# Kernel tuning notes

Measured on AMD Instinct MI355X. Metric: run time of the kernel, lower is better.

Reference implementation:

```python
import jax, jax.numpy as jnp
import numpy as np

NSAMPLE = 3  # three_nn default
EPS = 1e-10
CLAMP = 10.0


def setup_inputs() -> dict:
    key = jax.random.key(0)
    k1, k2, k3 = jax.random.split(key, 3)
    B, C, N = 4, 3, 8192
    pos1 = jax.random.normal(k1, (B, C, N), dtype=jnp.float32)
    pos2 = jax.random.normal(k2, (B, C, N), dtype=jnp.float32)
    flow1 = jax.random.normal(k3, (B, C, N), dtype=jnp.float32) * 0.1
    return {"pos1": pos1, "pos2": pos2, "flow1": flow1}


def reference(pos1, pos2, flow1):
    # pos1, flow1: [B,3,N1]; pos2: [B,3,N2]
    pos1_to_2 = pos1 + flow1                       # warped source points [B,3,N1]
    q = jnp.transpose(pos2, (0, 2, 1))             # queries  [B,N2,3]
    k = jnp.transpose(pos1_to_2, (0, 2, 1))        # database [B,N1,3]

    # brute-force 3-NN: squared distances [B,N2,N1]
    d2 = (jnp.sum(q * q, axis=-1, keepdims=True)
          - 2.0 * jnp.einsum('bqc,bnc->bqn', q, k)
          + jnp.sum(k * k, axis=-1)[:, None, :])
    _, knn_idx = jax.lax.top_k(-d2, NSAMPLE)       # [B,N2,NSAMPLE] into N1

    # gather neighbor coords: [B,N2,NSAMPLE,3]
    grouped_pts = jax.vmap(lambda pts, ii: pts[ii])(k, knn_idx)
    diff = grouped_pts - q[:, :, None, :]
    dist = jnp.maximum(jnp.linalg.norm(diff, axis=-1), EPS)  # [B,N2,NSAMPLE]
    inv = 1.0 / dist
    weight = inv / jnp.sum(inv, axis=-1, keepdims=True)      # [B,N2,NSAMPLE]

    # gather neighbor flows and do inverse-distance-weighted average
    flow_t = jnp.transpose(flow1, (0, 2, 1))                 # [B,N1,3]
    grouped_flow = jax.vmap(lambda f, ii: f[ii])(flow_t, knn_idx)  # [B,N2,NSAMPLE,3]
    flow2 = jnp.sum(weight[..., None] * grouped_flow, axis=2)      # [B,N2,3]

    warped = pos2 - jnp.transpose(flow2, (0, 2, 1))          # [B,3,N2]
    return jnp.clip(warped, -CLAMP, CLAMP)
```

## Files before the change

### kernel.cpp

```cpp
#include <hip/hip_runtime.h>
#include <math.h>


#define BB 4
#define NN 8192
#define NC 30
#define NCELLS (NC * NC * NC)
#define NCT (BB * NCELLS)
#define GRID_R 3.3f
#define GRID_INVH (1.0f / 0.22f)
#define D3_THR (0.44f * 0.44f * 0.999f)
#define EPB 1024
#define SB 106
#define NZ4 ((NCT + 4) / 4)

typedef unsigned long long u64;

__device__ __forceinline__ int cell_of(float x) {
  int c = (int)floorf((x + GRID_R) * GRID_INVH);
  return min(max(c, 0), NC - 1);
}

__device__ __forceinline__ void merge3(u64& a0, u64& a1, u64& a2,
                                       u64 b0, u64 b1, u64 b2) {
  const u64 lo0 = a0 < b0 ? a0 : b0;
  const u64 hi0 = a0 < b0 ? b0 : a0;
  const u64 lo1 = a1 < b1 ? a1 : b1;
  const u64 lo2 = a2 < b2 ? a2 : b2;
  const u64 o1 = hi0 < lo1 ? hi0 : lo1;
  const u64 t = hi0 < lo1 ? lo1 : hi0;
  a0 = lo0;
  a1 = o1;
  a2 = t < lo2 ? t : lo2;
}

__device__ __forceinline__ void insert3(u64& s0, u64& s1, u64& s2, u64 key) {
  const bool c0 = key < s0;
  const bool c1 = key < s1;
  const bool c2 = key < s2;
  s2 = c1 ? s1 : (c2 ? key : s2);
  s1 = c0 ? s0 : (c1 ? key : s1);
  s0 = c0 ? key : s0;
}

__device__ __forceinline__ void wave_merge3(u64& s0, u64& s1, u64& s2) {
#pragma unroll
  for (int mask = 32; mask >= 1; mask >>= 1) {
    const u64 b0 = __shfl_xor(s0, mask, 64);
    const u64 b1 = __shfl_xor(s1, mask, 64);
    const u64 b2 = __shfl_xor(s2, mask, 64);
    merge3(s0, s1, s2, b0, b1, b2);
  }
}

__device__ __forceinline__ void idw_out(int b, int qn, float qx, float qy,
                                        float qz, u64 s0, u64 s1, u64 s2,
                                        const float* __restrict__ P1,
                                        const float* __restrict__ F1,
                                        float* __restrict__ out) {
  const int idxs[3] = {(int)(unsigned)s0 & (NN - 1),
                       (int)(unsigned)s1 & (NN - 1),
                       (int)(unsigned)s2 & (NN - 1)};
  float w[3], gfx[3], gfy[3], gfz[3];
  float wsumv = 0.0f;
#pragma unroll
  for (int r = 0; r < 3; ++r) {
    const int idx = idxs[r];
    const float fx = F1[idx], fy = F1[NN + idx], fz = F1[2 * NN + idx];
    const float kx = P1[idx] + fx;
    const float ky = P1[NN + idx] + fy;
    const float kz = P1[2 * NN + idx] + fz;
    const float dx = kx - qx, dy = ky - qy, dz = kz - qz;
    float d = sqrtf(dx * dx + dy * dy + dz * dz);
    d = fmaxf(d, 1e-10f);
    const float inv = 1.0f / d;
    w[r] = inv; wsumv += inv;
    gfx[r] = fx; gfy[r] = fy; gfz[r] = fz;
  }
  const float invw = 1.0f / wsumv;
  float ox = 0.0f, oy = 0.0f, oz = 0.0f;
#pragma unroll
  for (int r = 0; r < 3; ++r) {
    const float ww = w[r] * invw;
    ox = fmaf(ww, gfx[r], ox);
    oy = fmaf(ww, gfy[r], oy);
    oz = fmaf(ww, gfz[r], oz);
  }
  ox = qx - ox; oy = qy - oy; oz = qz - oz;
  ox = fminf(fmaxf(ox, -10.0f), 10.0f);
  oy = fminf(fmaxf(oy, -10.0f), 10.0f);
  oz = fminf(fmaxf(oz, -10.0f), 10.0f);
  float* o = out + (size_t)b * 3 * NN;
  o[qn] = ox;
  o[NN + qn] = oy;
  o[2 * NN + qn] = oz;
}

__global__ __launch_bounds__(256) void k_zero(int4* __restrict__ p) {
  const int i = blockIdx.x * 256 + threadIdx.x;
  if (i < NZ4) p[i] = make_int4(0, 0, 0, 0);
}

__global__ __launch_bounds__(256) void k_count(const float* __restrict__ p1,
                                               const float* __restrict__ f1,
                                               int* __restrict__ counts) {
  const int gid = blockIdx.x * 256 + threadIdx.x;
  const int b = gid >> 13, n = gid & (NN - 1);
  const float* P = p1 + (size_t)b * 3 * NN;
  const float* F = f1 + (size_t)b * 3 * NN;
  const float x = P[n] + F[n];
  const float y = P[NN + n] + F[NN + n];
  const float z = P[2 * NN + n] + F[2 * NN + n];
  const int cid = (cell_of(z) * NC + cell_of(y)) * NC + cell_of(x);
  atomicAdd(&counts[b * NCELLS + cid], 1);
}

__global__ __launch_bounds__(256) void k_scan1(int* __restrict__ counts,
                                               int* __restrict__ offs,
                                               int* __restrict__ partials) {
  __shared__ int wsums[4];
  const int tid = threadIdx.x, lane = tid & 63, wav = tid >> 6;
  const int c = blockIdx.x * EPB + tid * 4;
  int4 v = make_int4(0, 0, 0, 0);
  if (c < NCT) {
    v = *reinterpret_cast<const int4*>(counts + c);
    *reinterpret_cast<int4*>(counts + c) = make_int4(0, 0, 0, 0);
  }
  const int sum4 = v.x + v.y + v.z + v.w;
  int incl = sum4;
  for (int off = 1; off < 64; off <<= 1) {
    const int t = __shfl_up(incl, off, 64);
    incl += (lane >= off) ? t : 0;
  }
  if (lane == 63) wsums[wav] = incl;
  __syncthreads();
  int wbase = 0;
#pragma unroll
  for (int w = 0; w < 4; ++w) wbase += (w < wav) ? wsums[w] : 0;
  const int excl = wbase + incl - sum4;
  if (c < NCT) {
    int4 e;
    e.x = excl;
    e.y = excl + v.x;
    e.z = e.y + v.y;
    e.w = e.z + v.z;
    *reinterpret_cast<int4*>(offs + c) = e;
  }
  if (tid == 255) partials[blockIdx.x] = wbase + incl;
}

__global__ __launch_bounds__(256) void k_finalize(int* __restrict__ offs,
                                                  const int* __restrict__ partials) {
  __shared__ int sbase;
  const int tid = threadIdx.x, lane = tid & 63;
  const int bid = blockIdx.x;
  if (tid < 64) {
    int v = 0;
    if (lane < bid) v = partials[lane];
    if (lane + 64 < bid) v += partials[lane + 64];
    for (int off = 32; off >= 1; off >>= 1) v += __shfl_down(v, off, 64);
    if (lane == 0) sbase = v;
  }
  __syncthreads();
  const int base = sbase;
  const int c = bid * EPB + tid * 4;
  if (c < NCT) {
    int4 v = *reinterpret_cast<const int4*>(offs + c);
    v.x += base; v.y += base; v.z += base; v.w += base;
    *reinterpret_cast<int4*>(offs + c) = v;
  }
  if (bid == 0 && tid == 0) offs[NCT] = BB * NN;
}

__global__ __launch_bounds__(256) void k_scatter(const float* __restrict__ p1,
                                                 const float* __restrict__ f1,
                                                 int* __restrict__ counts,
                                                 const int* __restrict__ offs,
                                                 float4* __restrict__ csr) {
  const int gid = blockIdx.x * 256 + threadIdx.x;
  const int b = gid >> 13, n = gid & (NN - 1);
  const float* P = p1 + (size_t)b * 3 * NN;
  const float* F = f1 + (size_t)b * 3 * NN;
  const float x = P[n] + F[n];
  const float y = P[NN + n] + F[NN + n];
  const float z = P[2 * NN + n] + F[2 * NN + n];
  const int cid = (cell_of(z) * NC + cell_of(y)) * NC + cell_of(x);
  const int g = b * NCELLS + cid;
  const int rank = atomicAdd(&counts[g], 1);
  csr[offs[g] + rank] = make_float4(x, y, z, __int_as_float(n));
}

__device__ __forceinline__ void col_range(int c, int qcy, int qcz, int cb,
                                          int gxl, int span,
                                          const int* __restrict__ offs,
                                          int& st, int& en) {
  const int dzi = (c * 205) >> 10;
  const int gz = qcz + dzi - 2;
  const int gy = qcy + (c - dzi * 5) - 2;
  st = 0; en = 0;
  if (((unsigned)gz < NC) & ((unsigned)gy < NC)) {
    const int ia = cb + (gz * NC + gy) * NC + gxl;
    st = offs[ia];
    en = offs[ia + span];
  }
}

__device__ __forceinline__ void cand1(const float4& a, float qx, float qy,
                                      float qz, u64& s0, u64& s1, u64& s2) {
  const float dx = a.x - qx, dy = a.y - qy, dz = a.z - qz;
  const float d2 = fmaf(dx, dx, fmaf(dy, dy, dz * dz));
  insert3(s0, s1, s2,
          ((u64)__float_as_uint(d2) << 32) | (unsigned)__float_as_uint(a.w));
}

__device__ __forceinline__ void scan_col(int st, int en,
                                         const float4* __restrict__ csr,
                                         float qx, float qy, float qz,
                                         u64& s0, u64& s1, u64& s2) {
  int j = st;
  for (; j + 4 <= en; j += 4) {
    const float4 a = csr[j];
    const float4 b = csr[j + 1];
    const float4 c = csr[j + 2];
    const float4 d = csr[j + 3];
    cand1(a, qx, qy, qz, s0, s1, s2);
    cand1(b, qx, qy, qz, s0, s1, s2);
    cand1(c, qx, qy, qz, s0, s1, s2);
    cand1(d, qx, qy, qz, s0, s1, s2);
  }
  for (; j < en; ++j) {
    const float4 a = csr[j];
    cand1(a, qx, qy, qz, s0, s1, s2);
  }
}

__global__ __launch_bounds__(256) void k_query(const float* __restrict__ p1,
                                               const float* __restrict__ p2,
                                               const float* __restrict__ f1,
                                               const int* __restrict__ offs,
                                               const float4* __restrict__ csr,
                                               float* __restrict__ out,
                                               int* __restrict__ fbcnt,
                                               int* __restrict__ fbq) {
  const int gtid = blockIdx.x * 256 + threadIdx.x;
  const int qid = gtid >> 4;
  const int r = gtid & 15;
  const int b = qid >> 13;
  const int qn = qid & (NN - 1);
  const float* P1 = p1 + (size_t)b * 3 * NN;
  const float* P2 = p2 + (size_t)b * 3 * NN;
  const float* F1 = f1 + (size_t)b * 3 * NN;

  const float qx = P2[qn], qy = P2[NN + qn], qz = P2[2 * NN + qn];
  const bool oor = !(fabsf(qx) < GRID_R && fabsf(qy) < GRID_R && fabsf(qz) < GRID_R);

  u64 s0 = ~0ULL, s1 = ~0ULL, s2 = ~0ULL;

  if (!oor) {
    const int qcx = cell_of(qx), qcy = cell_of(qy), qcz = cell_of(qz);
    const int gxl = max(qcx - 2, 0);
    const int span = min(qcx + 2, NC - 1) - gxl + 1;
    const int cb = b * NCELLS;

    int st0, en0, st1 = 0, en1 = 0;
    col_range(r, qcy, qcz, cb, gxl, span, offs, st0, en0);
    if (r < 9) col_range(r + 16, qcy, qcz, cb, gxl, span, offs, st1, en1);

    scan_col(st0, en0, csr, qx, qy, qz, s0, s1, s2);
    scan_col(st1, en1, csr, qx, qy, qz, s0, s1, s2);
  }

#pragma unroll
  for (int mask = 1; mask <= 8; mask <<= 1) {
    const u64 b0 = __shfl_xor(s0, mask, 64);
    const u64 b1 = __shfl_xor(s1, mask, 64);
    const u64 b2 = __shfl_xor(s2, mask, 64);
    merge3(s0, s1, s2, b0, b1, b2);
  }

  if (r == 0) {
    const float d3 = __uint_as_float((unsigned)(s2 >> 32));
    const bool ok = !oor && (d3 <= D3_THR);
    if (!ok) {
      const int slot = atomicAdd(&fbcnt[b], 1);
      fbq[b * NN + slot] = qn;
    } else {
      idw_out(b, qn, qx, qy, qz, s0, s1, s2, P1, F1, out);
    }
  }
}

__global__ __launch_bounds__(256) void k_fallback(const float* __restrict__ p1,
                                                  const float* __restrict__ p2,
                                                  const float* __restrict__ f1,
                                                  const int* __restrict__ fbcnt,
                                                  const int* __restrict__ fbq,
                                                  float* __restrict__ out) {
  __shared__ u64 redA[4][3];
  __shared__ u64 redC[4][3];
  const int b = blockIdx.y;
  const int nfb = fbcnt[b];
  const int tid = threadIdx.x, lane = tid & 63, wav = tid >> 6;
  const float* P1 = p1 + (size_t)b * 3 * NN;
  const float* P2 = p2 + (size_t)b * 3 * NN;
  const float* F1 = f1 + (size_t)b * 3 * NN;
  const int* q = fbq + b * NN;

  for (int base = blockIdx.x * 2; base < nfb; base += gridDim.x * 2) {
    const bool v1 = base + 1 < nfb;
    const int qn0 = q[base] & (NN - 1);
    const int qn1 = (v1 ? q[base + 1] : q[base]) & (NN - 1);
    const float q0x = P2[qn0], q0y = P2[NN + qn0], q0z = P2[2 * NN + qn0];
    const float q1x = P2[qn1], q1y = P2[NN + qn1], q1z = P2[2 * NN + qn1];

    u64 a0 = ~0ULL, a1 = ~0ULL, a2 = ~0ULL;
    u64 c0 = ~0ULL, c1 = ~0ULL, c2 = ~0ULL;

    for (int g0 = 0; g0 < NN; g0 += 1024) {
      const int g = g0 + tid;
      float xs[4], ys[4], zs[4];
#pragma unroll
      for (int k = 0; k < 4; ++k) {
        const int gg = g + k * 256;
        xs[k] = P1[gg] + F1[gg];
        ys[k] = P1[NN + gg] + F1[NN + gg];
        zs[k] = P1[2 * NN + gg] + F1[2 * NN + gg];
      }
#pragma unroll
      for (int k = 0; k < 4; ++k) {
        const unsigned gg = (unsigned)(g + k * 256);
        {
          const float dx = xs[k] - q0x, dy = ys[k] - q0y, dz = zs[k] - q0z;
          const float d2 = fmaf(dx, dx, fmaf(dy, dy, dz * dz));
          insert3(a0, a1, a2, ((u64)__float_as_uint(d2) << 32) | gg);
        }
        {
          const float dx = xs[k] - q1x, dy = ys[k] - q1y, dz = zs[k] - q1z;
          const float d2 = fmaf(dx, dx, fmaf(dy, dy, dz * dz));
          insert3(c0, c1, c2, ((u64)__float_as_uint(d2) << 32) | gg);
        }
      }
    }

    wave_merge3(a0, a1, a2);
    wave_merge3(c0, c1, c2);
    if (lane == 0) {
      redA[wav][0] = a0; redA[wav][1] = a1; redA[wav][2] = a2;
      redC[wav][0] = c0; redC[wav][1] = c1; redC[wav][2] = c2;
    }
    __syncthreads();
    if (tid == 0) {
      u64 m0 = redA[0][0], m1 = redA[0][1], m2 = redA[0][2];
#pragma unroll
      for (int w = 1; w < 4; ++w) merge3(m0, m1, m2, redA[w][0], redA[w][1], redA[w][2]);
      idw_out(b, qn0, q0x, q0y, q0z, m0, m1, m2, P1, F1, out);
    }
    if (tid == 1 && v1) {
      u64 m0 = redC[0][0], m1 = redC[0][1], m2 = redC[0][2];
#pragma unroll
      for (int w = 1; w < 4; ++w) merge3(m0, m1, m2, redC[w][0], redC[w][1], redC[w][2]);
      idw_out(b, qn1, q1x, q1y, q1z, m0, m1, m2, P1, F1, out);
    }
    __syncthreads();
  }
}

extern "C" void kernel_launch(void* const* d_in, const int* in_sizes, int n_in,
                              void* d_out, int out_size, void* d_ws, size_t ws_size,
                              hipStream_t stream) {
  const float* pos1 = (const float*)d_in[0];
  const float* pos2 = (const float*)d_in[1];
  const float* flow1 = (const float*)d_in[2];
  float* out = (float*)d_out;

  char* ws = (char*)d_ws;
  int* counts = (int*)ws;
  int* fbcnt = counts + NCT;
  size_t offs_off = (((size_t)NCT + 4) * 4 + 15) & ~(size_t)15;
  int* offs = (int*)(ws + offs_off);
  size_t part_off = (offs_off + ((size_t)NCT + 1) * 4 + 15) & ~(size_t)15;
  int* partials = (int*)(ws + part_off);
  size_t fbq_off = (part_off + (size_t)SB * 4 + 15) & ~(size_t)15;
  int* fbq = (int*)(ws + fbq_off);
  size_t csr_off = (fbq_off + (size_t)BB * NN * 4 + 15) & ~(size_t)15;
  float4* csr = (float4*)(ws + csr_off);

  k_zero<<<dim3((NZ4 + 255) / 256), dim3(256), 0, stream>>>((int4*)counts);
  k_count<<<dim3(BB * NN / 256), dim3(256), 0, stream>>>(pos1, flow1, counts);
  k_scan1<<<dim3(SB), dim3(256), 0, stream>>>(counts, offs, partials);
  k_finalize<<<dim3(SB), dim3(256), 0, stream>>>(offs, partials);
  k_scatter<<<dim3(BB * NN / 256), dim3(256), 0, stream>>>(pos1, flow1, counts, offs, csr);
  k_query<<<dim3(BB * NN * 16 / 256), dim3(256), 0, stream>>>(pos1, pos2, flow1, offs, csr, out, fbcnt, fbq);
  k_fallback<<<dim3(128, BB), dim3(256), 0, stream>>>(pos1, pos2, flow1, fbcnt, fbq, out);
}
```

Baseline: 70.97 us.

## Sort queries by grid cell so neighboring threads share CSR cells

Query points are binned into the same spatial grid as the database points through a shared count/scan/scatter pipeline, which produces a cell-sorted query list. k_query now reads its query id from this list, so adjacent waves process spatially nearby queries. The aim is better cache locality and less divergence in loop trip counts during the cell scans. The cost is a doubled scan array, more work in the count and scatter kernels, and an extra indirection per query.

Result: slower. 72.50 us (+2.1%).

```diff
diff --git a/kernel.cpp b/kernel.cpp
--- a/kernel.cpp
+++ b/kernel.cpp
@@ -4,15 +4,17 @@
 
 #define BB 4
 #define NN 8192
+#define BBNN (BB * NN)
 #define NC 30
 #define NCELLS (NC * NC * NC)
 #define NCT (BB * NCELLS)
+#define NCT2 (2 * NCT)
 #define GRID_R 3.3f
 #define GRID_INVH (1.0f / 0.22f)
 #define D3_THR (0.44f * 0.44f * 0.999f)
 #define EPB 1024
-#define SB 106
-#define NZ4 ((NCT + 4) / 4)
+#define SB 211
+#define NZ4 (NCT2 / 4 + 1)
 
 typedef unsigned long long u64;
 
@@ -51,6 +53,14 @@
     const u64 b2 = __shfl_xor(s2, mask, 64);
     merge3(s0, s1, s2, b0, b1, b2);
   }
+}
+
+__device__ __forceinline__ void cand1(const float4& a, float qx, float qy,
+                                      float qz, u64& s0, u64& s1, u64& s2) {
+  const float dx = a.x - qx, dy = a.y - qy, dz = a.z - qz;
+  const float d2 = fmaf(dx, dx, fmaf(dy, dy, dz * dz));
+  insert3(s0, s1, s2,
+          ((u64)__float_as_uint(d2) << 32) | (unsigned)__float_as_uint(a.w));
 }
 
 __device__ __forceinline__ void idw_out(int b, int qn, float qx, float qy,
@@ -102,17 +112,25 @@
 }
 
 __global__ __launch_bounds__(256) void k_count(const float* __restrict__ p1,
+                                               const float* __restrict__ p2,
                                                const float* __restrict__ f1,
                                                int* __restrict__ counts) {
   const int gid = blockIdx.x * 256 + threadIdx.x;
-  const int b = gid >> 13, n = gid & (NN - 1);
-  const float* P = p1 + (size_t)b * 3 * NN;
-  const float* F = f1 + (size_t)b * 3 * NN;
-  const float x = P[n] + F[n];
-  const float y = P[NN + n] + F[NN + n];
-  const float z = P[2 * NN + n] + F[2 * NN + n];
+  const bool isq = gid >= BBNN;
+  const int id = isq ? gid - BBNN : gid;
+  const int b = id >> 13, n = id & (NN - 1);
+  float x, y, z;
+  if (isq) {
+    const float* P = p2 + (size_t)b * 3 * NN;
+    x = P[n]; y = P[NN + n]; z = P[2 * NN + n];
+  } else {
+    const float* P = p1 + (size_t)b * 3 * NN;
+    const float* F = f1 + (size_t)b * 3 * NN;
+    x = P[n] + F[n]; y = P[NN + n] + F[NN + n]; z = P[2 * NN + n] + F[2 * NN + n];
+  }
   const int cid = (cell_of(z) * NC + cell_of(y)) * NC + cell_of(x);
-  atomicAdd(&counts[b * NCELLS + cid], 1);
+  const int g = (isq ? NCT : 0) + b * NCELLS + cid;
+  atomicAdd(&counts[g], 1);
 }
 
 __global__ __launch_bounds__(256) void k_scan1(int* __restrict__ counts,
@@ -122,7 +140,7 @@
   const int tid = threadIdx.x, lane = tid & 63, wav = tid >> 6;
   const int c = blockIdx.x * EPB + tid * 4;
   int4 v = make_int4(0, 0, 0, 0);
-  if (c < NCT) {
+  if (c < NCT2) {
     v = *reinterpret_cast<const int4*>(counts + c);
     *reinterpret_cast<int4*>(counts + c) = make_int4(0, 0, 0, 0);
   }
@@ -138,7 +156,7 @@
 #pragma unroll
   for (int w = 0; w < 4; ++w) wbase += (w < wav) ? wsums[w] : 0;
   const int excl = wbase + incl - sum4;
-  if (c < NCT) {
+  if (c < NCT2) {
     int4 e;
     e.x = excl;
     e.y = excl + v.x;
@@ -149,45 +167,58 @@
   if (tid == 255) partials[blockIdx.x] = wbase + incl;
 }
 
-__global__ __launch_bounds__(256) void k_finalize(int* __restrict__ offs,
-                                                  const int* __restrict__ partials) {
+__global__ __launch_bounds__(256) void k_final(int* __restrict__ offs,
+                                               const int* __restrict__ partials) {
   __shared__ int sbase;
   const int tid = threadIdx.x, lane = tid & 63;
   const int bid = blockIdx.x;
   if (tid < 64) {
     int v = 0;
-    if (lane < bid) v = partials[lane];
-    if (lane + 64 < bid) v += partials[lane + 64];
+#pragma unroll
+    for (int k = 0; k < 4; ++k) {
+      const int j = lane + 64 * k;
+      if (j < bid) v += partials[j];
+    }
     for (int off = 32; off >= 1; off >>= 1) v += __shfl_down(v, off, 64);
     if (lane == 0) sbase = v;
   }
   __syncthreads();
   const int base = sbase;
   const int c = bid * EPB + tid * 4;
-  if (c < NCT) {
+  if (c < NCT2) {
     int4 v = *reinterpret_cast<const int4*>(offs + c);
     v.x += base; v.y += base; v.z += base; v.w += base;
     *reinterpret_cast<int4*>(offs + c) = v;
   }
-  if (bid == 0 && tid == 0) offs[NCT] = BB * NN;
-}
-
-__global__ __launch_bounds__(256) void k_scatter(const float* __restrict__ p1,
-                                                 const float* __restrict__ f1,
-                                                 int* __restrict__ counts,
-                                                 const int* __restrict__ offs,
-                                                 float4* __restrict__ csr) {
+  if (bid == 0 && tid == 0) offs[NCT2] = 2 * BBNN;
+}
+
+__global__ __launch_bounds__(256) void k_scat(const float* __restrict__ p1,
+                                              const float* __restrict__ p2,
+                                              const float* __restrict__ f1,
+                                              int* __restrict__ counts,
+                                              const int* __restrict__ offs,
+                                              float4* __restrict__ csr,
+                                              int* __restrict__ qlist) {
   const int gid = blockIdx.x * 256 + threadIdx.x;
-  const int b = gid >> 13, n = gid & (NN - 1);
-  const float* P = p1 + (size_t)b * 3 * NN;
-  const float* F = f1 + (size_t)b * 3 * NN;
-  const float x = P[n] + F[n];
-  const float y = P[NN + n] + F[NN + n];
-  const float z = P[2 * NN + n] + F[2 * NN + n];
+  const bool isq = gid >= BBNN;
+  const int id = isq ? gid - BBNN : gid;
+  const int b = id >> 13, n = id & (NN - 1);
+  float x, y, z;
+  if (isq) {
+    const float* P = p2 + (size_t)b * 3 * NN;
+    x = P[n]; y = P[NN + n]; z = P[2 * NN + n];
+  } else {
+    const float* P = p1 + (size_t)b * 3 * NN;
+    const float* F = f1 + (size_t)b * 3 * NN;
+    x = P[n] + F[n]; y = P[NN + n] + F[NN + n]; z = P[2 * NN + n] + F[2 * NN + n];
+  }
   const int cid = (cell_of(z) * NC + cell_of(y)) * NC + cell_of(x);
-  const int g = b * NCELLS + cid;
+  const int g = (isq ? NCT : 0) + b * NCELLS + cid;
   const int rank = atomicAdd(&counts[g], 1);
-  csr[offs[g] + rank] = make_float4(x, y, z, __int_as_float(n));
+  const int pos = offs[g] + rank;
+  if (isq) qlist[pos - BBNN] = id;
+  else csr[pos] = make_float4(x, y, z, __int_as_float(n));
 }
 
 __device__ __forceinline__ void col_range(int c, int qcy, int qcz, int cb,
@@ -203,14 +234,6 @@
     st = offs[ia];
     en = offs[ia + span];
   }
-}
-
-__device__ __forceinline__ void cand1(const float4& a, float qx, float qy,
-                                      float qz, u64& s0, u64& s1, u64& s2) {
-  const float dx = a.x - qx, dy = a.y - qy, dz = a.z - qz;
-  const float d2 = fmaf(dx, dx, fmaf(dy, dy, dz * dz));
-  insert3(s0, s1, s2,
-          ((u64)__float_as_uint(d2) << 32) | (unsigned)__float_as_uint(a.w));
 }
 
 __device__ __forceinline__ void scan_col(int st, int en,
@@ -239,12 +262,14 @@
                                                const float* __restrict__ f1,
                                                const int* __restrict__ offs,
                                                const float4* __restrict__ csr,
+                                               const int* __restrict__ qlist,
                                                float* __restrict__ out,
                                                int* __restrict__ fbcnt,
                                                int* __restrict__ fbq) {
   const int gtid = blockIdx.x * 256 + threadIdx.x;
-  const int qid = gtid >> 4;
+  const int e = gtid >> 4;
   const int r = gtid & 15;
+  const int qid = qlist[e];
   const int b = qid >> 13;
   const int qn = qid & (NN - 1);
   const float* P1 = p1 + (size_t)b * 3 * NN;
@@ -375,21 +400,25 @@
 
   char* ws = (char*)d_ws;
   int* counts = (int*)ws;
-  int* fbcnt = counts + NCT;
-  size_t offs_off = (((size_t)NCT + 4) * 4 + 15) & ~(size_t)15;
+  int* fbcnt = counts + NCT2;
+  size_t offs_off = (((size_t)NCT2 + 4) * 4 + 15) & ~(size_t)15;
   int* offs = (int*)(ws + offs_off);
-  size_t part_off = (offs_off + ((size_t)NCT + 1) * 4 + 15) & ~(size_t)15;
+  size_t part_off = (offs_off + ((size_t)NCT2 + 1) * 4 + 15) & ~(size_t)15;
   int* partials = (int*)(ws + part_off);
-  size_t fbq_off = (part_off + (size_t)SB * 4 + 15) & ~(size_t)15;
+  size_t ql_off = (part_off + (size_t)SB * 4 + 15) & ~(size_t)15;
+  int* qlist = (int*)(ws + ql_off);
+  size_t fbq_off = (ql_off + (size_t)BBNN * 4 + 15) & ~(size_t)15;
   int* fbq = (int*)(ws + fbq_off);
-  size_t csr_off = (fbq_off + (size_t)BB * NN * 4 + 15) & ~(size_t)15;
+  size_t csr_off = (fbq_off + (size_t)BBNN * 4 + 15) & ~(size_t)15;
   float4* csr = (float4*)(ws + csr_off);
 
   k_zero<<<dim3((NZ4 + 255) / 256), dim3(256), 0, stream>>>((int4*)counts);
-  k_count<<<dim3(BB * NN / 256), dim3(256), 0, stream>>>(pos1, flow1, counts);
+  k_count<<<dim3(2 * BBNN / 256), dim3(256), 0, stream>>>(pos1, pos2, flow1, counts);
   k_scan1<<<dim3(SB), dim3(256), 0, stream>>>(counts, offs, partials);
-  k_finalize<<<dim3(SB), dim3(256), 0, stream>>>(offs, partials);
-  k_scatter<<<dim3(BB * NN / 256), dim3(256), 0, stream>>>(pos1, flow1, counts, offs, csr);
-  k_query<<<dim3(BB * NN * 16 / 256), dim3(256), 0, stream>>>(pos1, pos2, flow1, offs, csr, out, fbcnt, fbq);
+  k_final<<<dim3(SB), dim3(256), 0, stream>>>(offs, partials);
+  k_scat<<<dim3(2 * BBNN / 256), dim3(256), 0, stream>>>(pos1, pos2, flow1, counts,
+                                                         offs, csr, qlist);
+  k_query<<<dim3(BBNN * 16 / 256), dim3(256), 0, stream>>>(pos1, pos2, flow1, offs,
+                                                           csr, qlist, out, fbcnt, fbq);
   k_fallback<<<dim3(128, BB), dim3(256), 0, stream>>>(pos1, pos2, flow1, fbcnt, fbq, out);
 }
```

## Fuse scan passes via decoupled look-back and use 32 lanes per query

Applied to the files above, without the earlier changes.

Merges the two-pass block scan and finalize kernels into one kernel that resolves block prefixes with a decoupled look-back on per-block status words, removing a launch and a re-read and re-write of the offsets array. Separately, the query kernel now assigns 32 lanes per query, each scanning one of the 25 neighbour columns, instead of 16 lanes handling up to two columns each. This shortens the per-lane serial work at the cost of more threads, 7 idle lanes per query, and an extra shuffle-merge round. The look-back relies on all 106 scan blocks being co-resident to avoid spinning forever.

After: 71.05 us. Within noise of the previous version (+0.1%).

```diff
diff --git a/kernel.cpp b/kernel.cpp
--- a/kernel.cpp
+++ b/kernel.cpp
@@ -4,6 +4,7 @@
 
 #define BB 4
 #define NN 8192
+#define BBNN (BB * NN)
 #define NC 30
 #define NCELLS (NC * NC * NC)
 #define NCT (BB * NCELLS)
@@ -12,7 +13,10 @@
 #define D3_THR (0.44f * 0.44f * 0.999f)
 #define EPB 1024
 #define SB 106
-#define NZ4 ((NCT + 4) / 4)
+#define NZ4 ((NCT + 108 + 4) / 4)
+#define ST_PART 0x40000000u
+#define ST_DONE 0x80000000u
+#define ST_VAL 0x3FFFFFFFu
 
 typedef unsigned long long u64;
 
@@ -51,6 +55,14 @@
     const u64 b2 = __shfl_xor(s2, mask, 64);
     merge3(s0, s1, s2, b0, b1, b2);
   }
+}
+
+__device__ __forceinline__ void cand1(const float4& a, float qx, float qy,
+                                      float qz, u64& s0, u64& s1, u64& s2) {
+  const float dx = a.x - qx, dy = a.y - qy, dz = a.z - qz;
+  const float d2 = fmaf(dx, dx, fmaf(dy, dy, dz * dz));
+  insert3(s0, s1, s2,
+          ((u64)__float_as_uint(d2) << 32) | (unsigned)__float_as_uint(a.w));
 }
 
 __device__ __forceinline__ void idw_out(int b, int qn, float qx, float qy,
@@ -115,12 +127,14 @@
   atomicAdd(&counts[b * NCELLS + cid], 1);
 }
 
-__global__ __launch_bounds__(256) void k_scan1(int* __restrict__ counts,
-                                               int* __restrict__ offs,
-                                               int* __restrict__ partials) {
+__global__ __launch_bounds__(256) void k_scan(int* __restrict__ counts,
+                                              int* __restrict__ offs,
+                                              unsigned* __restrict__ scanst) {
   __shared__ int wsums[4];
+  __shared__ int sbase;
   const int tid = threadIdx.x, lane = tid & 63, wav = tid >> 6;
-  const int c = blockIdx.x * EPB + tid * 4;
+  const int bid = blockIdx.x;
+  const int c = bid * EPB + tid * 4;
   int4 v = make_int4(0, 0, 0, 0);
   if (c < NCT) {
     v = *reinterpret_cast<const int4*>(counts + c);
@@ -137,7 +151,40 @@
   int wbase = 0;
 #pragma unroll
   for (int w = 0; w < 4; ++w) wbase += (w < wav) ? wsums[w] : 0;
-  const int excl = wbase + incl - sum4;
+  const int btot = wsums[0] + wsums[1] + wsums[2] + wsums[3];
+
+  if (wav == 0) {
+    if (lane == 0) atomicExch(&scanst[bid], ST_PART | (unsigned)btot);
+    int base = 0;
+    int j0 = bid;
+    while (j0 > 0) {
+      const int j = j0 - 64 + lane;
+      unsigned s;
+      if (j >= 0) {
+        do { s = atomicAdd(&scanst[j], 0u); } while (s == 0u);
+      } else {
+        s = ST_DONE;
+      }
+      const u64 dball = __ballot((s & ST_DONE) != 0);
+      int val;
+      if (dball) {
+        const int hi = 63 - __clzll(dball);
+        val = (lane >= hi) ? (int)(s & ST_VAL) : 0;
+      } else {
+        val = (int)(s & ST_VAL);
+      }
+      for (int off = 32; off >= 1; off >>= 1) val += __shfl_down(val, off, 64);
+      base += __shfl(val, 0, 64);
+      if (dball) break;
+      j0 -= 64;
+    }
+    if (lane == 0) {
+      atomicExch(&scanst[bid], ST_DONE | (unsigned)(base + btot));
+      sbase = base;
+    }
+  }
+  __syncthreads();
+  const int excl = sbase + wbase + incl - sum4;
   if (c < NCT) {
     int4 e;
     e.x = excl;
@@ -146,37 +193,14 @@
     e.w = e.z + v.z;
     *reinterpret_cast<int4*>(offs + c) = e;
   }
-  if (tid == 255) partials[blockIdx.x] = wbase + incl;
-}
-
-__global__ __launch_bounds__(256) void k_finalize(int* __restrict__ offs,
-                                                  const int* __restrict__ partials) {
-  __shared__ int sbase;
-  const int tid = threadIdx.x, lane = tid & 63;
-  const int bid = blockIdx.x;
-  if (tid < 64) {
-    int v = 0;
-    if (lane < bid) v = partials[lane];
-    if (lane + 64 < bid) v += partials[lane + 64];
-    for (int off = 32; off >= 1; off >>= 1) v += __shfl_down(v, off, 64);
-    if (lane == 0) sbase = v;
-  }
-  __syncthreads();
-  const int base = sbase;
-  const int c = bid * EPB + tid * 4;
-  if (c < NCT) {
-    int4 v = *reinterpret_cast<const int4*>(offs + c);
-    v.x += base; v.y += base; v.z += base; v.w += base;
-    *reinterpret_cast<int4*>(offs + c) = v;
-  }
-  if (bid == 0 && tid == 0) offs[NCT] = BB * NN;
-}
-
-__global__ __launch_bounds__(256) void k_scatter(const float* __restrict__ p1,
-                                                 const float* __restrict__ f1,
-                                                 int* __restrict__ counts,
-                                                 const int* __restrict__ offs,
-                                                 float4* __restrict__ csr) {
+  if (bid == SB - 1 && tid == 0) offs[NCT] = BBNN;
+}
+
+__global__ __launch_bounds__(256) void k_scat(const float* __restrict__ p1,
+                                              const float* __restrict__ f1,
+                                              int* __restrict__ counts,
+                                              const int* __restrict__ offs,
+                                              float4* __restrict__ csr) {
   const int gid = blockIdx.x * 256 + threadIdx.x;
   const int b = gid >> 13, n = gid & (NN - 1);
   const float* P = p1 + (size_t)b * 3 * NN;
@@ -188,29 +212,6 @@
   const int g = b * NCELLS + cid;
   const int rank = atomicAdd(&counts[g], 1);
   csr[offs[g] + rank] = make_float4(x, y, z, __int_as_float(n));
-}
-
-__device__ __forceinline__ void col_range(int c, int qcy, int qcz, int cb,
-                                          int gxl, int span,
-                                          const int* __restrict__ offs,
-                                          int& st, int& en) {
-  const int dzi = (c * 205) >> 10;
-  const int gz = qcz + dzi - 2;
-  const int gy = qcy + (c - dzi * 5) - 2;
-  st = 0; en = 0;
-  if (((unsigned)gz < NC) & ((unsigned)gy < NC)) {
-    const int ia = cb + (gz * NC + gy) * NC + gxl;
-    st = offs[ia];
-    en = offs[ia + span];
-  }
-}
-
-__device__ __forceinline__ void cand1(const float4& a, float qx, float qy,
-                                      float qz, u64& s0, u64& s1, u64& s2) {
-  const float dx = a.x - qx, dy = a.y - qy, dz = a.z - qz;
-  const float d2 = fmaf(dx, dx, fmaf(dy, dy, dz * dz));
-  insert3(s0, s1, s2,
-          ((u64)__float_as_uint(d2) << 32) | (unsigned)__float_as_uint(a.w));
 }
 
 __device__ __forceinline__ void scan_col(int st, int en,
@@ -243,8 +244,8 @@
                                                int* __restrict__ fbcnt,
                                                int* __restrict__ fbq) {
   const int gtid = blockIdx.x * 256 + threadIdx.x;
-  const int qid = gtid >> 4;
-  const int r = gtid & 15;
+  const int qid = gtid >> 5;
+  const int r = gtid & 31;
   const int b = qid >> 13;
   const int qn = qid & (NN - 1);
   const float* P1 = p1 + (size_t)b * 3 * NN;
@@ -256,22 +257,23 @@
 
   u64 s0 = ~0ULL, s1 = ~0ULL, s2 = ~0ULL;
 
-  if (!oor) {
+  if (!oor && r < 25) {
     const int qcx = cell_of(qx), qcy = cell_of(qy), qcz = cell_of(qz);
     const int gxl = max(qcx - 2, 0);
     const int span = min(qcx + 2, NC - 1) - gxl + 1;
-    const int cb = b * NCELLS;
-
-    int st0, en0, st1 = 0, en1 = 0;
-    col_range(r, qcy, qcz, cb, gxl, span, offs, st0, en0);
-    if (r < 9) col_range(r + 16, qcy, qcz, cb, gxl, span, offs, st1, en1);
-
-    scan_col(st0, en0, csr, qx, qy, qz, s0, s1, s2);
-    scan_col(st1, en1, csr, qx, qy, qz, s0, s1, s2);
-  }
-
-#pragma unroll
-  for (int mask = 1; mask <= 8; mask <<= 1) {
+    const int dzi = (r * 205) >> 10;
+    const int gz = qcz + dzi - 2;
+    const int gy = qcy + (r - dzi * 5) - 2;
+    if (((unsigned)gz < NC) & ((unsigned)gy < NC)) {
+      const int ia = b * NCELLS + (gz * NC + gy) * NC + gxl;
+      const int st = offs[ia];
+      const int en = offs[ia + span];
+      scan_col(st, en, csr, qx, qy, qz, s0, s1, s2);
+    }
+  }
+
+#pragma unroll
+  for (int mask = 1; mask <= 16; mask <<= 1) {
     const u64 b0 = __shfl_xor(s0, mask, 64);
     const u64 b1 = __shfl_xor(s1, mask, 64);
     const u64 b2 = __shfl_xor(s2, mask, 64);
@@ -375,21 +377,20 @@
 
   char* ws = (char*)d_ws;
   int* counts = (int*)ws;
-  int* fbcnt = counts + NCT;
-  size_t offs_off = (((size_t)NCT + 4) * 4 + 15) & ~(size_t)15;
+  unsigned* scanst = (unsigned*)(counts + NCT);
+  int* fbcnt = (int*)(counts + NCT + 108);
+  size_t offs_off = (size_t)(NCT + 112) * 4;
   int* offs = (int*)(ws + offs_off);
-  size_t part_off = (offs_off + ((size_t)NCT + 1) * 4 + 15) & ~(size_t)15;
-  int* partials = (int*)(ws + part_off);
-  size_t fbq_off = (part_off + (size_t)SB * 4 + 15) & ~(size_t)15;
+  size_t fbq_off = (offs_off + ((size_t)NCT + 1) * 4 + 15) & ~(size_t)15;
   int* fbq = (int*)(ws + fbq_off);
-  size_t csr_off = (fbq_off + (size_t)BB * NN * 4 + 15) & ~(size_t)15;
+  size_t csr_off = (fbq_off + (size_t)BBNN * 4 + 15) & ~(size_t)15;
   float4* csr = (float4*)(ws + csr_off);
 
   k_zero<<<dim3((NZ4 + 255) / 256), dim3(256), 0, stream>>>((int4*)counts);
-  k_count<<<dim3(BB * NN / 256), dim3(256), 0, stream>>>(pos1, flow1, counts);
-  k_scan1<<<dim3(SB), dim3(256), 0, stream>>>(counts, offs, partials);
-  k_finalize<<<dim3(SB), dim3(256), 0, stream>>>(offs, partials);
-  k_scatter<<<dim3(BB * NN / 256), dim3(256), 0, stream>>>(pos1, flow1, counts, offs, csr);
-  k_query<<<dim3(BB * NN * 16 / 256), dim3(256), 0, stream>>>(pos1, pos2, flow1, offs, csr, out, fbcnt, fbq);
+  k_count<<<dim3(BBNN / 256), dim3(256), 0, stream>>>(pos1, flow1, counts);
+  k_scan<<<dim3(SB), dim3(256), 0, stream>>>(counts, offs, scanst);
+  k_scat<<<dim3(BBNN / 256), dim3(256), 0, stream>>>(pos1, flow1, counts, offs, csr);
+  k_query<<<dim3(BBNN * 32 / 256), dim3(256), 0, stream>>>(pos1, pos2, flow1, offs,
+                                                           csr, out, fbcnt, fbq);
   k_fallback<<<dim3(128, BB), dim3(256), 0, stream>>>(pos1, pos2, flow1, fbcnt, fbq, out);
 }
```
